# Kernel tuning notes

Hardware: AMD Instinct MI355X
Metric: run time of the kernel (lower is better)

The kernel has to match this reference:

```python
import jax, jax.numpy as jnp
import numpy as np

DIM, QK, PDIM = 256, 16, 64
EPS = 1e-5  # BatchNorm2d / GroupNorm default eps
SCALE = QK ** -0.5


def bn_eval(y, w, b, rm, rv):
    # eval-mode BatchNorm2d folded to per-channel scale+shift
    inv = w / jnp.sqrt(rv + EPS)
    return y * inv[None, :, None, None] + (b - rm * inv)[None, :, None, None]


def setup_inputs() -> dict:
    key = jax.random.key(0)
    ks = jax.random.split(key, 14)
    qkv_out = 2 * QK + PDIM  # 96
    d = {}
    d["x"] = jax.random.normal(ks[0], (4, DIM, 64, 64), jnp.float32)
    # GroupNorm(1, pdim) affine params
    d["gn_w"] = 1.0 + 0.1 * jax.random.normal(ks[1], (PDIM,), jnp.float32)
    d["gn_b"] = 0.1 * jax.random.normal(ks[2], (PDIM,), jnp.float32)
    # qkv Conv2d_BN: 1x1 conv (no bias) + BN
    d["qkv_w"] = 0.05 * jax.random.normal(ks[3], (qkv_out, PDIM), jnp.float32)
    d["qkv_bn_w"] = 1.0 + 0.1 * jax.random.normal(ks[4], (qkv_out,), jnp.float32)
    d["qkv_bn_b"] = 0.1 * jax.random.normal(ks[5], (qkv_out,), jnp.float32)
    d["qkv_rm"] = 0.1 * jax.random.normal(ks[6], (qkv_out,), jnp.float32)
    d["qkv_rv"] = jax.random.uniform(ks[7], (qkv_out,), jnp.float32, 0.5, 1.5)
    # proj Conv2d_BN: 1x1 conv (no bias) + BN (bn_weight_init=0 in torch; use random for nontrivial output)
    d["proj_w"] = 0.05 * jax.random.normal(ks[8], (DIM, DIM), jnp.float32)
    d["proj_bn_w"] = 1.0 + 0.1 * jax.random.normal(ks[9], (DIM,), jnp.float32)
    d["proj_bn_b"] = 0.1 * jax.random.normal(ks[10], (DIM,), jnp.float32)
    d["proj_rm"] = 0.1 * jax.random.normal(ks[11], (DIM,), jnp.float32)
    d["proj_rv"] = jax.random.uniform(ks[12], (DIM,), jnp.float32, 0.5, 1.5)
    return d


def reference(x, gn_w, gn_b, qkv_w, qkv_bn_w, qkv_bn_b, qkv_rm, qkv_rv,
              proj_w, proj_bn_w, proj_bn_b, proj_rm, proj_rv):
    B, C, H, W = x.shape
    N = H * W
    x1, x2 = x[:, :PDIM], x[:, PDIM:]
    # GroupNorm with 1 group: normalize over (C, H, W) per sample
    mu = jnp.mean(x1, axis=(1, 2, 3), keepdims=True)
    var = jnp.var(x1, axis=(1, 2, 3), keepdims=True)
    x1n = (x1 - mu) * jax.lax.rsqrt(var + EPS)
    x1n = x1n * gn_w[None, :, None, None] + gn_b[None, :, None, None]
    # 1x1 conv + BN (eval)
    qkv = bn_eval(jnp.einsum('bchw,oc->bohw', x1n, qkv_w),
                  qkv_bn_w, qkv_bn_b, qkv_rm, qkv_rv)
    q = qkv[:, :QK].reshape(B, QK, N)
    k = qkv[:, QK:2 * QK].reshape(B, QK, N)
    v = qkv[:, 2 * QK:].reshape(B, PDIM, N)
    # attn[b, n, m] = sum_c q[b,c,n] * k[b,c,m]
    attn = jnp.einsum('bcn,bcm->bnm', q, k) * SCALE
    attn = jax.nn.softmax(attn, axis=-1)
    # x1 = v @ attn^T : out[b,p,n] = sum_m v[b,p,m] * attn[b,n,m]
    x1o = jnp.einsum('bpm,bnm->bpn', v, attn).reshape(B, PDIM, H, W)
    y = jnp.concatenate([x1o, x2], axis=1)
    y = jax.nn.silu(y)
    y = bn_eval(jnp.einsum('bchw,oc->bohw', y, proj_w),
                proj_bn_w, proj_bn_b, proj_rm, proj_rv)
    return y
```

## Files before the change

### kernel.cpp

```cpp
#include <hip/hip_runtime.h>
#include <hip/hip_bf16.h>
#include <math.h>

static constexpr int B_ = 4;
static constexpr int C_ = 256;
static constexpr int PD_ = 64;
static constexpr int N_ = 4096;
static constexpr int O96_ = 96;
static constexpr float EPS_ = 1e-5f;
static constexpr float SCALE_ = 0.25f;
static constexpr float LOG2E_ = 1.4426950408889634f;

typedef __attribute__((ext_vector_type(8))) short short8v;
typedef __attribute__((ext_vector_type(4))) float f32x4;

__device__ inline short f2bf(float x) {
    __hip_bfloat16 h = __float2bfloat16(x);
    short r; __builtin_memcpy(&r, &h, 2); return r;
}
__device__ inline float bf2f(short s) {
    union { float f; unsigned u; } v; v.u = ((unsigned)(unsigned short)s) << 16;
    return v.f;
}
__device__ inline unsigned pack_bf2(float lo, float hi) {
    return ((unsigned)(unsigned short)f2bf(hi) << 16) | (unsigned)(unsigned short)f2bf(lo);
}
__device__ inline float silu_(float v) { return v / (1.0f + __expf(-v)); }
__device__ inline float exp2_fast(float x) {
#if __has_builtin(__builtin_amdgcn_exp2f)
    return __builtin_amdgcn_exp2f(x);
#else
    return __expf(x * 0.6931471805599453f);
#endif
}

__global__ __launch_bounds__(256) void k_gnw(const float* __restrict__ x,
        float* __restrict__ part,
        const float* __restrict__ pw,  const float* __restrict__ bnw,
        const float* __restrict__ bnb, const float* __restrict__ rm,
        const float* __restrict__ rv,  short* __restrict__ wbf,
        float* __restrict__ beta) {
    if (blockIdx.x >= 256) {
        const int idx = (blockIdx.x - 256) * 256 + threadIdx.x;
        const int o = idx >> 8, c = idx & 255;
        const float inv = bnw[o] * rsqrtf(rv[o] + EPS_);
        wbf[idx] = f2bf(pw[idx] * inv);
        if (c == 0) beta[o] = bnb[o] - rm[o] * inv;
        return;
    }
    const int blk = blockIdx.x;
    const int b = blk >> 6, c = blk & 63;
    const float* p = x + (size_t)(b * C_ + c) * N_;
    float s = 0.f, q = 0.f;
    for (int i = threadIdx.x; i < N_; i += 256) {
        float v = p[i]; s += v; q += v * v;
    }
    for (int d = 1; d < 64; d <<= 1) {
        s += __shfl_xor(s, d, 64);
        q += __shfl_xor(q, d, 64);
    }
    __shared__ float ls[4], lq[4];
    const int lane = threadIdx.x & 63, wid = threadIdx.x >> 6;
    if (lane == 0) { ls[wid] = s; lq[wid] = q; }
    __syncthreads();
    if (threadIdx.x == 0) {
        part[2 * blk]     = ls[0] + ls[1] + ls[2] + ls[3];
        part[2 * blk + 1] = lq[0] + lq[1] + lq[2] + lq[3];
    }
}

__global__ __launch_bounds__(512) void k_qkv(const float* __restrict__ x,
        const float* __restrict__ gnw, const float* __restrict__ gnb,
        const float* __restrict__ qw,  const float* __restrict__ bnw,
        const float* __restrict__ bnb, const float* __restrict__ rm,
        const float* __restrict__ rv,  const float* __restrict__ part,
        short* __restrict__ qT, short* __restrict__ kfrag, short* __restrict__ vfrag) {
    __shared__ float wl[O96_ * PD_];
    __shared__ float binv[O96_], bbeta[O96_];
    __shared__ float musr[2];
    const int t = threadIdx.x;
    const int b = blockIdx.x >> 6;
    const int n0 = (blockIdx.x & 63) << 6;
    if (t < 64) {
        float s = part[2 * (b * 64 + t)];
        float q = part[2 * (b * 64 + t) + 1];
        for (int d = 1; d < 64; d <<= 1) {
            s += __shfl_xor(s, d, 64);
            q += __shfl_xor(q, d, 64);
        }
        if (t == 0) {
            const float inv_n = 1.0f / (float)(PD_ * N_);
            float mu = s * inv_n;
            float var = q * inv_n - mu * mu;
            musr[0] = mu;
            musr[1] = rsqrtf(var + EPS_);
        }
    }
    for (int i = t; i < O96_ * PD_; i += 512) wl[i] = qw[i];
    for (int o = t; o < O96_; o += 512) {
        float inv  = bnw[o] * rsqrtf(rv[o] + EPS_);
        float beta = bnb[o] - rm[o] * inv;
        if (o < 16) { inv *= SCALE_ * LOG2E_; beta *= SCALE_ * LOG2E_; }
        binv[o] = inv; bbeta[o] = beta;
    }
    __syncthreads();
    const float mu = musr[0], rs = musr[1];
    const int nl = t & 63;
    const int n  = n0 + nl;
    const int og = t >> 6;
    float xn[PD_];
    const float* xb = x + (size_t)b * C_ * N_ + n;
    #pragma unroll
    for (int c = 0; c < PD_; ++c)
        xn[c] = (xb[(size_t)c * N_] - mu) * rs * gnw[c] + gnb[c];
    const size_t mblk = (size_t)b * 64 + (n >> 6);
    short* qrow = qT + ((size_t)b * N_ + n) * 16;
    short* kbase = kfrag + mblk * 1024;
    short* vbase = vfrag + mblk * 4096;
    const int mtk  = 2 * ((nl >> 2) & 1) + (nl >> 5);
    const int colk = 4 * ((nl >> 3) & 3) + (nl & 3);
    const int ks = nl >> 5, gv = (nl >> 3) & 3, jv = nl & 7;
    for (int o = og * 12; o < og * 12 + 12; ++o) {
        const float4* wr = (const float4*)&wl[o * PD_];
        float a = 0.f;
        #pragma unroll
        for (int c4 = 0; c4 < 16; ++c4) {
            float4 w4 = wr[c4];
            a += w4.x * xn[4*c4] + w4.y * xn[4*c4+1] + w4.z * xn[4*c4+2] + w4.w * xn[4*c4+3];
        }
        short val = f2bf(a * binv[o] + bbeta[o]);
        if (o < 16) {
            qrow[o] = val;
        } else if (o < 32) {
            const int c = o - 16;
            kbase[((mtk * 2 + (c >> 3)) * 16 + colk) * 8 + (c & 7)] = val;
        } else {
            const int p = o - 32;
            vbase[(((ks * 4 + (p >> 4)) * 64) + gv * 16 + (p & 15)) * 8 + jv] = val;
        }
    }
}

__global__ __launch_bounds__(256) void k_attn(const short* __restrict__ qT,
        const short* __restrict__ kfrag, const short* __restrict__ vfrag,
        short* __restrict__ apart) {
    const int wg  = blockIdx.x;
    const int swz = (wg & 7) * 128 + (wg >> 3);
    const int b   = swz >> 8;
    const int mq  = (swz >> 5) & 7;
    const int nt  = swz & 31;
    const int n0  = nt << 7;

    const int t    = threadIdx.x;
    const int w    = t >> 6;
    const int lane = t & 63;
    const int g    = lane >> 4;
    const int col  = lane & 15;

    const short* qbase = qT + ((size_t)b * N_ + n0 + w * 32 + col) * 16;
    const short* kfb = kfrag + ((size_t)b * 64 + mq * 8) * 1024;
    const short* vfb = vfrag + ((size_t)b * 64 + mq * 8) * 4096;

    short8v a_q0 = 0, a_q1 = 0;
    if (g < 2) {
        a_q0 = *(const short8v*)(qbase + 8 * g);
        a_q1 = *(const short8v*)(qbase + 256 + 8 * g);
    }
    short8v onesf = 0;
    if (col == 0) {
        #pragma unroll
        for (int j = 0; j < 8; ++j) onesf[j] = (short)0x3F80;
    }

    f32x4 acc0[5], acc1[5];
    #pragma unroll
    for (int pt = 0; pt < 5; ++pt) { acc0[pt] = 0.f; acc1[pt] = 0.f; }

    for (int it = 0; it < 8; ++it) {
        const short* kit = kfb + it * 1024;
        const short* vit = vfb + it * 4096;
        short8v kr[4];
        #pragma unroll
        for (int mt = 0; mt < 4; ++mt) {
            kr[mt] = 0;
            if (g < 2) kr[mt] = *(const short8v*)(kit + ((mt * 2 + g) * 16 + col) * 8);
        }
        short8v vpre[8];
        #pragma unroll
        for (int j = 0; j < 8; ++j)
            vpre[j] = *(const short8v*)(vit + (j * 64 + g * 16 + col) * 8);
        f32x4 s[4];
        #pragma unroll
        for (int mt = 0; mt < 4; ++mt) {
            f32x4 z = 0.f;
            s[mt] = __builtin_amdgcn_mfma_f32_16x16x32_bf16(kr[mt], a_q0, z, 0, 0, 0);
        }
        union { unsigned u[4]; short8v v; } p0k0, p0k1, p1k0, p1k1;
        p0k0.u[0] = pack_bf2(exp2_fast(s[0][0]), exp2_fast(s[0][1]));
        p0k0.u[1] = pack_bf2(exp2_fast(s[0][2]), exp2_fast(s[0][3]));
        p0k0.u[2] = pack_bf2(exp2_fast(s[2][0]), exp2_fast(s[2][1]));
        p0k0.u[3] = pack_bf2(exp2_fast(s[2][2]), exp2_fast(s[2][3]));
        p0k1.u[0] = pack_bf2(exp2_fast(s[1][0]), exp2_fast(s[1][1]));
        p0k1.u[1] = pack_bf2(exp2_fast(s[1][2]), exp2_fast(s[1][3]));
        p0k1.u[2] = pack_bf2(exp2_fast(s[3][0]), exp2_fast(s[3][1]));
        p0k1.u[3] = pack_bf2(exp2_fast(s[3][2]), exp2_fast(s[3][3]));
        #pragma unroll
        for (int mt = 0; mt < 4; ++mt) {
            f32x4 z = 0.f;
            s[mt] = __builtin_amdgcn_mfma_f32_16x16x32_bf16(kr[mt], a_q1, z, 0, 0, 0);
        }
        p1k0.u[0] = pack_bf2(exp2_fast(s[0][0]), exp2_fast(s[0][1]));
        p1k0.u[1] = pack_bf2(exp2_fast(s[0][2]), exp2_fast(s[0][3]));
        p1k0.u[2] = pack_bf2(exp2_fast(s[2][0]), exp2_fast(s[2][1]));
        p1k0.u[3] = pack_bf2(exp2_fast(s[2][2]), exp2_fast(s[2][3]));
        p1k1.u[0] = pack_bf2(exp2_fast(s[1][0]), exp2_fast(s[1][1]));
        p1k1.u[1] = pack_bf2(exp2_fast(s[1][2]), exp2_fast(s[1][3]));
        p1k1.u[2] = pack_bf2(exp2_fast(s[3][0]), exp2_fast(s[3][1]));
        p1k1.u[3] = pack_bf2(exp2_fast(s[3][2]), exp2_fast(s[3][3]));
        acc0[4] = __builtin_amdgcn_mfma_f32_16x16x32_bf16(p0k0.v, onesf, acc0[4], 0, 0, 0);
        acc0[4] = __builtin_amdgcn_mfma_f32_16x16x32_bf16(p0k1.v, onesf, acc0[4], 0, 0, 0);
        acc1[4] = __builtin_amdgcn_mfma_f32_16x16x32_bf16(p1k0.v, onesf, acc1[4], 0, 0, 0);
        acc1[4] = __builtin_amdgcn_mfma_f32_16x16x32_bf16(p1k1.v, onesf, acc1[4], 0, 0, 0);
        #pragma unroll
        for (int pt = 0; pt < 4; ++pt) {
            acc0[pt] = __builtin_amdgcn_mfma_f32_16x16x32_bf16(p0k0.v, vpre[pt],     acc0[pt], 0, 0, 0);
            acc0[pt] = __builtin_amdgcn_mfma_f32_16x16x32_bf16(p0k1.v, vpre[4 + pt], acc0[pt], 0, 0, 0);
            acc1[pt] = __builtin_amdgcn_mfma_f32_16x16x32_bf16(p1k0.v, vpre[pt],     acc1[pt], 0, 0, 0);
            acc1[pt] = __builtin_amdgcn_mfma_f32_16x16x32_bf16(p1k1.v, vpre[4 + pt], acc1[pt], 0, 0, 0);
        }
    }
    short* po = apart + (size_t)((b * 8 + mq) * 32 + nt) * 8448;
    #pragma unroll
    for (int pt = 0; pt < 4; ++pt) {
        #pragma unroll
        for (int r = 0; r < 4; ++r) {
            po[(w * 32 + 4 * g + r) * 64 + pt * 16 + col]      = f2bf(acc0[pt][r]);
            po[(w * 32 + 16 + 4 * g + r) * 64 + pt * 16 + col] = f2bf(acc1[pt][r]);
        }
    }
    if (col == 0) {
        float* ms = (float*)(po + 8192);
        #pragma unroll
        for (int r = 0; r < 4; ++r) {
            ms[w * 32 + 4 * g + r]      = acc0[4][r];
            ms[w * 32 + 16 + 4 * g + r] = acc1[4][r];
        }
    }
}

__global__ __launch_bounds__(256) void k_proj2(const short* __restrict__ apart,
        const float* __restrict__ x, const short* __restrict__ wbf,
        const float* __restrict__ beta, float* __restrict__ out) {
    __shared__ __align__(16) short ybf[32 * 256];
    const int t  = threadIdx.x;
    const int nt = blockIdx.x;
    const int b  = blockIdx.y;
    const int n0 = nt << 5;

    {
        const int nn = t >> 3, pg = t & 7;
        const int qloc = ((nt & 3) << 5) + nn;
        const short* pbase = apart + (size_t)((b * 8) * 32 + (nt >> 2)) * 8448;
        float oacc[8] = {0.f, 0.f, 0.f, 0.f, 0.f, 0.f, 0.f, 0.f};
        float Ssum = 0.f;
        #pragma unroll
        for (int k = 0; k < 8; ++k) {
            const short* pk = pbase + (size_t)k * 32 * 8448;
            Ssum += ((const float*)(pk + 8192))[qloc];
            short8v a = *(const short8v*)(pk + qloc * 64 + pg * 8);
            #pragma unroll
            for (int j = 0; j < 8; ++j) oacc[j] += bf2f(a[j]);
        }
        const float inv = 1.0f / Ssum;
        const int slot = pg ^ (nn & 7);
        *(uint4*)(ybf + nn * 256 + slot * 8) = make_uint4(
            pack_bf2(silu_(oacc[0] * inv), silu_(oacc[1] * inv)),
            pack_bf2(silu_(oacc[2] * inv), silu_(oacc[3] * inv)),
            pack_bf2(silu_(oacc[4] * inv), silu_(oacc[5] * inv)),
            pack_bf2(silu_(oacc[6] * inv), silu_(oacc[7] * inv)));
    }
    {
        const int nn = t & 31, cg = t >> 5;
        #pragma unroll
        for (int s3 = 0; s3 < 3; ++s3) {
            const int cb = 64 + cg * 24 + s3 * 8;
            unsigned pk4[4];
            #pragma unroll
            for (int j = 0; j < 4; ++j) {
                float v0 = x[((size_t)(b * C_ + cb + 2 * j)) * N_ + n0 + nn];
                float v1 = x[((size_t)(b * C_ + cb + 2 * j + 1)) * N_ + n0 + nn];
                pk4[j] = pack_bf2(silu_(v0), silu_(v1));
            }
            const int slot = (8 + cg * 3 + s3) ^ (nn & 7);
            *(uint4*)(ybf + nn * 256 + slot * 8) = make_uint4(pk4[0], pk4[1], pk4[2], pk4[3]);
        }
    }
    __syncthreads();
    const int w = t >> 6, lane = t & 63;
    const int col = lane & 15, g = lane >> 4;
    const int o_base = w << 6;
    f32x4 acc[4][2];
    #pragma unroll
    for (int ot = 0; ot < 4; ++ot) { acc[ot][0] = 0.f; acc[ot][1] = 0.f; }
    #pragma unroll
    for (int kk = 0; kk < 8; ++kk) {
        short8v bf0 = *(const short8v*)(ybf + col * 256 + (((kk * 4 + g) ^ (col & 7)) << 3));
        short8v bf1 = *(const short8v*)(ybf + (16 + col) * 256 + (((kk * 4 + g) ^ (col & 7)) << 3));
        #pragma unroll
        for (int ot = 0; ot < 4; ++ot) {
            short8v af = *(const short8v*)(wbf + (size_t)(o_base + ot * 16 + col) * C_ + kk * 32 + g * 8);
            acc[ot][0] = __builtin_amdgcn_mfma_f32_16x16x32_bf16(af, bf0, acc[ot][0], 0, 0, 0);
            acc[ot][1] = __builtin_amdgcn_mfma_f32_16x16x32_bf16(af, bf1, acc[ot][1], 0, 0, 0);
        }
    }
    #pragma unroll
    for (int ot = 0; ot < 4; ++ot) {
        #pragma unroll
        for (int r = 0; r < 4; ++r) {
            const int o = o_base + ot * 16 + 4 * g + r;
            const float be = beta[o];
            float* po = out + ((size_t)(b * C_ + o)) * N_ + n0 + col;
            po[0]  = acc[ot][0][r] + be;
            po[16] = acc[ot][1][r] + be;
        }
    }
}

extern "C" void kernel_launch(void* const* d_in, const int* in_sizes, int n_in,
                              void* d_out, int out_size, void* d_ws, size_t ws_size,
                              hipStream_t stream) {
    const float* x   = (const float*)d_in[0];
    const float* gnw = (const float*)d_in[1];
    const float* gnb = (const float*)d_in[2];
    const float* qw  = (const float*)d_in[3];
    const float* qbw = (const float*)d_in[4];
    const float* qbb = (const float*)d_in[5];
    const float* qrm = (const float*)d_in[6];
    const float* qrv = (const float*)d_in[7];
    const float* pw  = (const float*)d_in[8];
    const float* pbw = (const float*)d_in[9];
    const float* pbb = (const float*)d_in[10];
    const float* prm = (const float*)d_in[11];
    const float* prv = (const float*)d_in[12];
    float* out = (float*)d_out;
    char* wsb = (char*)d_ws;

    float* part  = (float*)wsb;
    short* wbf   = (short*)(wsb + 4096);
    float* beta  = (float*)(wsb + 135168);
    short* qTb   = (short*)(wsb + 139264);
    short* kfrag = (short*)(wsb + 663552);
    short* vfrag = (short*)(wsb + 1187840);
    short* apart = (short*)(wsb + 3284992);

    k_gnw<<<512, 256, 0, stream>>>(x, part, pw, pbw, pbb, prm, prv, wbf, beta);
    k_qkv<<<256, 512, 0, stream>>>(x, gnw, gnb, qw, qbw, qbb, qrm, qrv, part, qTb, kfrag, vfrag);
    k_attn<<<1024, 256, 0, stream>>>(qTb, kfrag, vfrag, apart);
    k_proj2<<<dim3(128, 4), 256, 0, stream>>>(apart, x, wbf, beta, out);
}
```

Measured before the change: 66.31 us.

## Compute QKV projection with bf16 MFMA and fold GroupNorm into weights

New measurement: 55.71 us (median of 2 runs). 1.19x faster.

```diff
diff --git a/kernel.cpp b/kernel.cpp
--- a/kernel.cpp
+++ b/kernel.cpp
@@ -50,10 +50,13 @@
     }
     const int blk = blockIdx.x;
     const int b = blk >> 6, c = blk & 63;
-    const float* p = x + (size_t)(b * C_ + c) * N_;
+    const float4* p4 = (const float4*)(x + (size_t)(b * C_ + c) * N_);
     float s = 0.f, q = 0.f;
-    for (int i = threadIdx.x; i < N_; i += 256) {
-        float v = p[i]; s += v; q += v * v;
+    #pragma unroll
+    for (int i = 0; i < 4; ++i) {
+        float4 v = p4[threadIdx.x + i * 256];
+        s += v.x + v.y + v.z + v.w;
+        q += v.x * v.x + v.y * v.y + v.z * v.z + v.w * v.w;
     }
     for (int d = 1; d < 64; d <<= 1) {
         s += __shfl_xor(s, d, 64);
@@ -75,8 +78,9 @@
         const float* __restrict__ bnb, const float* __restrict__ rm,
         const float* __restrict__ rv,  const float* __restrict__ part,
         short* __restrict__ qT, short* __restrict__ kfrag, short* __restrict__ vfrag) {
-    __shared__ float wl[O96_ * PD_];
-    __shared__ float binv[O96_], bbeta[O96_];
+    __shared__ __align__(16) short wfrag[6][2][512];
+    __shared__ __align__(16) short xfrag[64][64];
+    __shared__ float bias2[96];
     __shared__ float musr[2];
     const int t = threadIdx.x;
     const int b = blockIdx.x >> 6;
@@ -96,47 +100,79 @@
             musr[1] = rsqrtf(var + EPS_);
         }
     }
-    for (int i = t; i < O96_ * PD_; i += 512) wl[i] = qw[i];
-    for (int o = t; o < O96_; o += 512) {
-        float inv  = bnw[o] * rsqrtf(rv[o] + EPS_);
-        float beta = bnb[o] - rm[o] * inv;
-        if (o < 16) { inv *= SCALE_ * LOG2E_; beta *= SCALE_ * LOG2E_; }
-        binv[o] = inv; bbeta[o] = beta;
+    {
+        const int nq = t & 15, c0 = t >> 4;
+        #pragma unroll
+        for (int pass = 0; pass < 2; ++pass) {
+            const int c = c0 + pass * 32;
+            float4 v4 = *(const float4*)(x + ((size_t)(b * C_ + c)) * N_ + n0 + nq * 4);
+            const int c8 = c >> 3, cj = c & 7;
+            float vv[4] = {v4.x, v4.y, v4.z, v4.w};
+            #pragma unroll
+            for (int e = 0; e < 4; ++e) {
+                const int n = nq * 4 + e;
+                xfrag[n][((c8 ^ (n & 7)) << 3) + cj] = f2bf(vv[e]);
+            }
+        }
     }
     __syncthreads();
     const float mu = musr[0], rs = musr[1];
-    const int nl = t & 63;
-    const int n  = n0 + nl;
-    const int og = t >> 6;
-    float xn[PD_];
-    const float* xb = x + (size_t)b * C_ * N_ + n;
-    #pragma unroll
-    for (int c = 0; c < PD_; ++c)
-        xn[c] = (xb[(size_t)c * N_] - mu) * rs * gnw[c] + gnb[c];
-    const size_t mblk = (size_t)b * 64 + (n >> 6);
-    short* qrow = qT + ((size_t)b * N_ + n) * 16;
+    if (t < 96) {
+        const int o = t;
+        float inv  = bnw[o] * rsqrtf(rv[o] + EPS_);
+        float bet  = bnb[o] - rm[o] * inv;
+        if (o < 16) { inv *= SCALE_ * LOG2E_; bet *= SCALE_ * LOG2E_; }
+        const float* wr = qw + o * PD_;
+        const int ot = o >> 4, colo = o & 15;
+        float bacc = 0.f;
+        #pragma unroll
+        for (int c = 0; c < PD_; ++c) {
+            const float ga = rs * gnw[c];
+            const float gb = gnb[c] - mu * ga;
+            const float wv = wr[c];
+            bacc += wv * gb;
+            wfrag[ot][c >> 5][((((c >> 3) & 3) * 16 + colo) << 3) + (c & 7)] = f2bf(wv * ga * inv);
+        }
+        bias2[o] = bet + inv * bacc;
+    }
+    __syncthreads();
+    const int w = t >> 6, lane = t & 63;
+    const int col = lane & 15, g = lane >> 4;
+    const int nt2 = w & 3, oh = w >> 2;
+    const int nloc = nt2 * 16 + col;
+    short8v bf0 = *(const short8v*)(&xfrag[nloc][((0 + g) ^ (nloc & 7)) << 3]);
+    short8v bf1 = *(const short8v*)(&xfrag[nloc][((4 + g) ^ (nloc & 7)) << 3]);
+    const int n = n0 + nloc;
+    const int nl = nloc;
+    const size_t mblk = (size_t)b * 64 + (blockIdx.x & 63);
     short* kbase = kfrag + mblk * 1024;
     short* vbase = vfrag + mblk * 4096;
     const int mtk  = 2 * ((nl >> 2) & 1) + (nl >> 5);
     const int colk = 4 * ((nl >> 3) & 3) + (nl & 3);
     const int ks = nl >> 5, gv = (nl >> 3) & 3, jv = nl & 7;
-    for (int o = og * 12; o < og * 12 + 12; ++o) {
-        const float4* wr = (const float4*)&wl[o * PD_];
-        float a = 0.f;
-        #pragma unroll
-        for (int c4 = 0; c4 < 16; ++c4) {
-            float4 w4 = wr[c4];
-            a += w4.x * xn[4*c4] + w4.y * xn[4*c4+1] + w4.z * xn[4*c4+2] + w4.w * xn[4*c4+3];
-        }
-        short val = f2bf(a * binv[o] + bbeta[o]);
-        if (o < 16) {
-            qrow[o] = val;
-        } else if (o < 32) {
-            const int c = o - 16;
-            kbase[((mtk * 2 + (c >> 3)) * 16 + colk) * 8 + (c & 7)] = val;
+    #pragma unroll
+    for (int oi = 0; oi < 3; ++oi) {
+        const int ot = oh * 3 + oi;
+        short8v af0 = *(const short8v*)(&wfrag[ot][0][lane * 8]);
+        short8v af1 = *(const short8v*)(&wfrag[ot][1][lane * 8]);
+        f32x4 acc = 0.f;
+        acc = __builtin_amdgcn_mfma_f32_16x16x32_bf16(af0, bf0, acc, 0, 0, 0);
+        acc = __builtin_amdgcn_mfma_f32_16x16x32_bf16(af1, bf1, acc, 0, 0, 0);
+        if (ot == 0) {
+            unsigned lo = pack_bf2(acc[0] + bias2[4*g+0], acc[1] + bias2[4*g+1]);
+            unsigned hi = pack_bf2(acc[2] + bias2[4*g+2], acc[3] + bias2[4*g+3]);
+            *(uint2*)(qT + ((size_t)b * N_ + n) * 16 + 4 * g) = make_uint2(lo, hi);
+        } else if (ot == 1) {
+            unsigned lo = pack_bf2(acc[0] + bias2[16+4*g+0], acc[1] + bias2[16+4*g+1]);
+            unsigned hi = pack_bf2(acc[2] + bias2[16+4*g+2], acc[3] + bias2[16+4*g+3]);
+            *(uint2*)(kbase + (((mtk * 2 + (g >> 1)) * 16 + colk) << 3) + 4 * (g & 1)) = make_uint2(lo, hi);
         } else {
-            const int p = o - 32;
-            vbase[(((ks * 4 + (p >> 4)) * 64) + gv * 16 + (p & 15)) * 8 + jv] = val;
+            #pragma unroll
+            for (int r = 0; r < 4; ++r) {
+                const int o = ot * 16 + 4 * g + r;
+                vbase[(((ks * 4 + (ot - 2)) * 64 + gv * 16 + 4 * g + r) << 3) + jv] =
+                    f2bf(acc[r] + bias2[o]);
+            }
         }
     }
 }
```
